# Kernel tuning notes

Measured on AMD Instinct MI355X. Metric: run time of the kernel, lower is better.

Reference implementation:

```python
import jax, jax.numpy as jnp
import numpy as np

NUM_EMB = 1000
HIDDEN = 256
SCALE = 2
N_HEADS = 8
HEAD_DIM = HIDDEN * SCALE // N_HEADS  # 64
HS = HIDDEN * SCALE  # 512
EPS = 1e-6


def setup_inputs() -> dict:
    key = jax.random.key(0)
    ks = jax.random.split(key, 12)
    B, N, C, H, W = 8, 8, HIDDEN, 32, 32
    std = 0.02
    return {
        "q": jax.random.randint(ks[0], (B,), 0, NUM_EMB, dtype=jnp.int32),
        "c": jax.random.normal(ks[1], (B, N, C, H, W), dtype=jnp.float32),
        "rms_w": jnp.ones((HIDDEN,), dtype=jnp.float32),
        "emb": jax.random.normal(ks[2], (NUM_EMB, HIDDEN), dtype=jnp.float32) * std,
        "w1": jax.random.normal(ks[3], (HIDDEN, HS), dtype=jnp.float32) * std,
        "b1": jnp.zeros((HS,), dtype=jnp.float32),
        "w2": jax.random.normal(ks[4], (HS, HS), dtype=jnp.float32) * std,
        "b2": jnp.zeros((HS,), dtype=jnp.float32),
        "w_kv": jax.random.normal(ks[5], (HIDDEN, HS * 2), dtype=jnp.float32) * std,
        "w_out": jax.random.normal(ks[6], (HS, HIDDEN), dtype=jnp.float32) * std,
        "b_out": jnp.zeros((HIDDEN,), dtype=jnp.float32),
    }


def reference(q, c, rms_w, emb, w1, b1, w2, b2, w_kv, w_out, b_out):
    B, N, C, H, W = c.shape
    attn_scale = HEAD_DIM ** (-0.5)
    # permute to [B,H,W,N,C] and RMSNorm over channel dim
    c = jnp.transpose(c, (0, 3, 4, 1, 2))
    c = c * jax.lax.rsqrt(jnp.mean(c * c, axis=-1, keepdims=True) + EPS) * rms_w
    # query path: embed + gated MLP -> [B, n_heads, head_dim]
    qe = emb[q]                                   # [B, hidden]
    qh = jax.nn.silu(qe @ w1 + b1) @ w2 + b2      # [B, HS]
    qh = qh.reshape(B, N_HEADS, HEAD_DIM)
    # kv projection: [B,H,W,N, 2*HS] -> [B,H,W,n_heads,N, 2*head_dim]
    kv = (c @ w_kv).reshape(B, H, W, N, N_HEADS, 2 * HEAD_DIM)
    kv = jnp.transpose(kv, (0, 1, 2, 4, 3, 5))
    k, v = jnp.split(kv, 2, axis=-1)              # each [B,H,W,heads,N,head_dim]
    # broadcast per-pixel cross-attention: query shared over H,W
    dots = jnp.einsum('bed,bhwend->bhwen', qh, k) * attn_scale
    attn = jax.nn.softmax(dots, axis=-1)
    h = jnp.einsum('bhwen,bhwend->bhwed', attn, v)  # [B,H,W,heads,head_dim]
    h = h.reshape(B, H, W, HS)
    out = h @ w_out + b_out                        # [B,H,W,hidden]
    return jnp.transpose(out, (0, 3, 1, 2))        # [B,hidden,H,W]
```

## Files before the change

kernel.cpp:

```cpp
#include <hip/hip_runtime.h>

typedef _Float16 f16;
typedef _Float16 f16x4 __attribute__((ext_vector_type(4)));
typedef _Float16 f16x8 __attribute__((ext_vector_type(8)));
typedef float f32x4 __attribute__((ext_vector_type(4)));

static __device__ inline char* a_addr(char* Abase, int px, int k) {
    return Abase + px * 4096 + ((((k >> 3) ^ (px & 15)) << 4) | ((k & 7) << 1));
}

__launch_bounds__(256)
__global__ void k_setup(const int* __restrict__ q, const float* __restrict__ emb,
                        const float* __restrict__ w1, const float* __restrict__ b1,
                        const float* __restrict__ w2, const float* __restrict__ b2,
                        const float* __restrict__ w_kv, const float* __restrict__ w_out,
                        const float* __restrict__ rms_w,
                        f16* __restrict__ qkw, f16* __restrict__ mtp) {
    int blk = blockIdx.x;
    int t = threadIdx.x;
    __shared__ float qe[256];
    __shared__ float x1L[512];
    __shared__ float ps[4][64];
    __shared__ float qhL[64];
    __shared__ float wv[64][8];

    if (blk < 64) {
        int b = blk >> 3, e = blk & 7;
        qe[t] = emb[(size_t)q[b] * 256 + t];
        __syncthreads();
        float a0 = b1[t], a1 = b1[t + 256];
#pragma unroll 4
        for (int c = 0; c < 256; ++c) {
            float qv = qe[c];
            a0 += qv * w1[c * 512 + t];
            a1 += qv * w1[c * 512 + t + 256];
        }
        x1L[t]       = a0 / (1.f + __expf(-a0));
        x1L[t + 256] = a1 / (1.f + __expf(-a1));
        __syncthreads();
        int d = t & 63, ks = t >> 6;
        float acc = 0.f;
#pragma unroll 4
        for (int k = ks * 128; k < ks * 128 + 128; ++k)
            acc += x1L[k] * w2[k * 512 + e * 64 + d];
        ps[ks][d] = acc;
        __syncthreads();
        if (t < 64)
            qhL[t] = b2[e * 64 + t] + ps[0][t] + ps[1][t] + ps[2][t] + ps[3][t];
        __syncthreads();
        const float* row = w_kv + (size_t)t * 1024 + e * 128;
        float a2 = 0.f;
#pragma unroll
        for (int dd = 0; dd < 64; dd += 4) {
            float4 wv4 = *(const float4*)(row + dd);
            a2 += qhL[dd] * wv4.x + qhL[dd + 1] * wv4.y + qhL[dd + 2] * wv4.z + qhL[dd + 3] * wv4.w;
        }
        qkw[(b * 8 + e) * 256 + t] = (f16)(a2 * rms_w[t]);
    } else {
        int mb = blk - 64;
        int e = mb >> 5, c0 = (mb & 31) * 8;
        {
            int d = t & 63, cc = t >> 6;
            wv[d][cc]     = w_kv[(size_t)(c0 + cc) * 1024 + e * 128 + 64 + d];
            wv[d][cc + 4] = w_kv[(size_t)(c0 + cc + 4) * 1024 + e * 128 + 64 + d];
        }
        __syncthreads();
        int o = t;
        float acc[8];
#pragma unroll
        for (int c = 0; c < 8; ++c) acc[c] = 0.f;
#pragma unroll 4
        for (int d = 0; d < 64; ++d) {
            float wo = w_out[(size_t)(e * 64 + d) * 256 + o];
            float4 wa = *(const float4*)&wv[d][0];
            float4 wb = *(const float4*)&wv[d][4];
            acc[0] += wa.x * wo; acc[1] += wa.y * wo; acc[2] += wa.z * wo; acc[3] += wa.w * wo;
            acc[4] += wb.x * wo; acc[5] += wb.y * wo; acc[6] += wb.z * wo; acc[7] += wb.w * wo;
        }
        f16x8 ov;
#pragma unroll
        for (int c = 0; c < 8; ++c) ov[c] = (f16)(acc[c] * rms_w[c0 + c]);
        *(f16x8*)(mtp + ((size_t)((e * 256 + c0) >> 3) * 256 + o) * 8) = ov;
    }
}

__launch_bounds__(1024, 4)
__global__ void k_attn(const float* __restrict__ cin, const f16* __restrict__ qkw,
                       const f16* __restrict__ mtp, const float* __restrict__ b_out,
                       float* __restrict__ out) {
    int blk = blockIdx.x;
    int b = blk & 7;
    int hw0 = (blk >> 3) * 32;
    int t = threadIdx.x;
    int lane = t & 63, w = t >> 6;
    int m16 = lane & 15, quad = lane >> 4;
    int half = lane >> 5;

    __shared__ char A[32 * 4096];
    __shared__ float dotsP[8][8][32];
    __shared__ float wredS[16][16];
    __shared__ f16  attnH[8 * 32 * 8];

    int n = w & 7, pxh = w >> 3;
    int px = pxh * 16 + m16;
    {
        const float* cb0 = cin + (((size_t)b * 2048) << 10) + hw0 + px;
        int chb = n * 256 + quad * 64;
        float ss = 0.f;
#pragma unroll
        for (int g = 0; g < 4; ++g) {
            float v[16];
#pragma unroll
            for (int j = 0; j < 16; ++j)
                v[j] = cb0[(size_t)(chb + g * 16 + j) << 10];
            f16x8 h0, h1;
#pragma unroll
            for (int j = 0; j < 8; ++j) { ss += v[j] * v[j]; h0[j] = (f16)v[j]; }
#pragma unroll
            for (int j = 0; j < 8; ++j) { float x = v[8 + j]; ss += x * x; h1[j] = (f16)x; }
            *(f16x8*)a_addr(A, px, chb + g * 16)     = h0;
            *(f16x8*)a_addr(A, px, chb + g * 16 + 8) = h1;
        }
        ss += __shfl_xor(ss, 16);
        ss += __shfl_xor(ss, 32);
        if (lane < 16) wredS[w][m16] = ss;
    }
    {
        f32x4 d0 = {0.f, 0.f, 0.f, 0.f};
        const f16* qrow = qkw + (size_t)b * 2048 + (m16 & 7) * 256;
#pragma unroll
        for (int ks = 0; ks < 8; ++ks) {
            f16x8 a0 = *(const f16x8*)a_addr(A, px, n * 256 + ks * 32 + quad * 8);
            f16x8 bq = *(const f16x8*)(qrow + ks * 32 + quad * 8);
            d0 = __builtin_amdgcn_mfma_f32_16x16x32_f16(a0, bq, d0, 0, 0, 0);
        }
        if (m16 < 8) {
#pragma unroll
            for (int r = 0; r < 4; ++r) dotsP[n][m16][pxh * 16 + quad * 4 + r] = d0[r];
        }
    }
    __syncthreads();

    int o = w * 16 + m16;
    f16x8 pb[8];
#pragma unroll
    for (int ks = 0; ks < 8; ++ks)
        pb[ks] = *(const f16x8*)(mtp + ((size_t)(ks * 4 + quad) * 256 + o) * 8);

    if (t < 256) {
        int e = t >> 5, p = t & 31;
        int ph = p >> 4, pl = p & 15;
        float rv[8], l[8];
#pragma unroll
        for (int nn = 0; nn < 8; ++nn)
            rv[nn] = rsqrtf(wredS[ph * 8 + nn][pl] * (1.f / 256.f) + 1e-6f);
#pragma unroll
        for (int nn = 0; nn < 8; ++nn) l[nn] = dotsP[nn][e][p] * rv[nn] * 0.125f;
        float mx = l[0];
#pragma unroll
        for (int nn = 1; nn < 8; ++nn) mx = fmaxf(mx, l[nn]);
        float s = 0.f;
#pragma unroll
        for (int nn = 0; nn < 8; ++nn) { l[nn] = __expf(l[nn] - mx); s += l[nn]; }
        float inv = 1.f / s;
        f16x8 av;
#pragma unroll
        for (int nn = 0; nn < 8; ++nn) av[nn] = (f16)(l[nn] * inv * rv[nn]);
        *(f16x8*)(attnH + e * 256 + p * 8) = av;
    }
    __syncthreads();

    {
        int bpx = lane & 31;
        int c0 = (w + half * 16) * 8;
        f16x8 cv[8];
#pragma unroll
        for (int nn = 0; nn < 8; ++nn)
            cv[nn] = *(const f16x8*)a_addr(A, bpx, nn * 256 + c0);
#pragma unroll
        for (int e = 0; e < 8; ++e) {
            f16x8 av = *(const f16x8*)(attnH + e * 256 + bpx * 8);
            f16x8 r = {};
#pragma unroll
            for (int nn = 0; nn < 8; ++nn) {
                f16 an = av[nn];
#pragma unroll
                for (int j = 0; j < 8; ++j) r[j] += cv[nn][j] * an;
            }
            *(f16x8*)a_addr(A, bpx, e * 256 + c0) = r;
        }
    }
    __syncthreads();

    {
        f32x4 acc0 = {0.f, 0.f, 0.f, 0.f};
        f32x4 acc1 = {0.f, 0.f, 0.f, 0.f};
#pragma unroll
        for (int ks = 0; ks < 8; ++ks) {
            int k = ks * 32 + quad * 8;
            f16x8 af0 = *(const f16x8*)a_addr(A, m16, k);
            f16x8 af1 = *(const f16x8*)a_addr(A, m16 + 16, k);
            acc0 = __builtin_amdgcn_mfma_f32_16x16x32_f16(af0, pb[ks], acc0, 0, 0, 0);
            acc1 = __builtin_amdgcn_mfma_f32_16x16x32_f16(af1, pb[ks], acc1, 0, 0, 0);
        }
#pragma unroll 8
        for (int ks = 8; ks < 64; ++ks) {
            int k = (ks >> 3) * 256 + (ks & 7) * 32 + quad * 8;
            int kchunk = k >> 3;
            f16x8 bfr = *(const f16x8*)(mtp + ((size_t)kchunk * 256 + o) * 8);
            f16x8 af0 = *(const f16x8*)a_addr(A, m16, k);
            f16x8 af1 = *(const f16x8*)a_addr(A, m16 + 16, k);
            acc0 = __builtin_amdgcn_mfma_f32_16x16x32_f16(af0, bfr, acc0, 0, 0, 0);
            acc1 = __builtin_amdgcn_mfma_f32_16x16x32_f16(af1, bfr, acc1, 0, 0, 0);
        }
        float bo = b_out[o];
        float* drow = out + ((size_t)b * 256 + o) * 1024 + hw0;
        float4 v0 = {acc0[0] + bo, acc0[1] + bo, acc0[2] + bo, acc0[3] + bo};
        float4 v1 = {acc1[0] + bo, acc1[1] + bo, acc1[2] + bo, acc1[3] + bo};
        *(float4*)(drow + quad * 4)      = v0;
        *(float4*)(drow + 16 + quad * 4) = v1;
    }
}

extern "C" void kernel_launch(void* const* d_in, const int* in_sizes, int n_in,
                              void* d_out, int out_size, void* d_ws, size_t ws_size,
                              hipStream_t stream) {
    (void)in_sizes; (void)n_in; (void)out_size; (void)ws_size;
    const int*   q     = (const int*)d_in[0];
    const float* c     = (const float*)d_in[1];
    const float* rms_w = (const float*)d_in[2];
    const float* emb   = (const float*)d_in[3];
    const float* w1    = (const float*)d_in[4];
    const float* b1    = (const float*)d_in[5];
    const float* w2    = (const float*)d_in[6];
    const float* b2    = (const float*)d_in[7];
    const float* w_kv  = (const float*)d_in[8];
    const float* w_out = (const float*)d_in[9];
    const float* b_out = (const float*)d_in[10];
    float* out = (float*)d_out;

    char* ws = (char*)d_ws;
    f16* qkw = (f16*)ws;
    f16* mtp = (f16*)(ws + 32768);

    k_setup<<<320, 256, 0, stream>>>(q, emb, w1, b1, w2, b2, w_kv, w_out, rms_w, qkw, mtp);
    k_attn <<<256, 1024, 0, stream>>>(c, qkw, mtp, b_out, out);
}
```

Baseline: 168.0 us.

## Fuse setup into attention kernel with grid-wide flag barrier and overlapped loads

Merges the weight-preprocessing kernel into the attention kernel. The first four warps of each block compute the folded w_kv·w_out slice and, in 64 blocks, the query MLP chain. The remaining warps stream the input tile into shared memory at the same time. A global atomic counter barrier, reset by a memset, makes every block wait until all qkw and mtp data is published. The aim is to remove one launch and hide the setup latency behind the input loads. The cost is a grid-wide spin wait, which relies on all 256 blocks being co-resident, and fewer warps doing the input loads.

```diff
diff --git a/kernel.cpp b/kernel.cpp
--- a/kernel.cpp
+++ b/kernel.cpp
@@ -5,89 +5,23 @@
 typedef _Float16 f16x8 __attribute__((ext_vector_type(8)));
 typedef float f32x4 __attribute__((ext_vector_type(4)));
 
+#define WS_QKW   0
+#define WS_MTP   32768
+#define WS_FLAGS (32768 + 1048576)
+
 static __device__ inline char* a_addr(char* Abase, int px, int k) {
     return Abase + px * 4096 + ((((k >> 3) ^ (px & 15)) << 4) | ((k & 7) << 1));
 }
 
-__launch_bounds__(256)
-__global__ void k_setup(const int* __restrict__ q, const float* __restrict__ emb,
+__launch_bounds__(1024, 4)
+__global__ void k_fused(const int* __restrict__ q, const float* __restrict__ emb,
                         const float* __restrict__ w1, const float* __restrict__ b1,
                         const float* __restrict__ w2, const float* __restrict__ b2,
                         const float* __restrict__ w_kv, const float* __restrict__ w_out,
-                        const float* __restrict__ rms_w,
-                        f16* __restrict__ qkw, f16* __restrict__ mtp) {
-    int blk = blockIdx.x;
-    int t = threadIdx.x;
-    __shared__ float qe[256];
-    __shared__ float x1L[512];
-    __shared__ float ps[4][64];
-    __shared__ float qhL[64];
-    __shared__ float wv[64][8];
-
-    if (blk < 64) {
-        int b = blk >> 3, e = blk & 7;
-        qe[t] = emb[(size_t)q[b] * 256 + t];
-        __syncthreads();
-        float a0 = b1[t], a1 = b1[t + 256];
-#pragma unroll 4
-        for (int c = 0; c < 256; ++c) {
-            float qv = qe[c];
-            a0 += qv * w1[c * 512 + t];
-            a1 += qv * w1[c * 512 + t + 256];
-        }
-        x1L[t]       = a0 / (1.f + __expf(-a0));
-        x1L[t + 256] = a1 / (1.f + __expf(-a1));
-        __syncthreads();
-        int d = t & 63, ks = t >> 6;
-        float acc = 0.f;
-#pragma unroll 4
-        for (int k = ks * 128; k < ks * 128 + 128; ++k)
-            acc += x1L[k] * w2[k * 512 + e * 64 + d];
-        ps[ks][d] = acc;
-        __syncthreads();
-        if (t < 64)
-            qhL[t] = b2[e * 64 + t] + ps[0][t] + ps[1][t] + ps[2][t] + ps[3][t];
-        __syncthreads();
-        const float* row = w_kv + (size_t)t * 1024 + e * 128;
-        float a2 = 0.f;
-#pragma unroll
-        for (int dd = 0; dd < 64; dd += 4) {
-            float4 wv4 = *(const float4*)(row + dd);
-            a2 += qhL[dd] * wv4.x + qhL[dd + 1] * wv4.y + qhL[dd + 2] * wv4.z + qhL[dd + 3] * wv4.w;
-        }
-        qkw[(b * 8 + e) * 256 + t] = (f16)(a2 * rms_w[t]);
-    } else {
-        int mb = blk - 64;
-        int e = mb >> 5, c0 = (mb & 31) * 8;
-        {
-            int d = t & 63, cc = t >> 6;
-            wv[d][cc]     = w_kv[(size_t)(c0 + cc) * 1024 + e * 128 + 64 + d];
-            wv[d][cc + 4] = w_kv[(size_t)(c0 + cc + 4) * 1024 + e * 128 + 64 + d];
-        }
-        __syncthreads();
-        int o = t;
-        float acc[8];
-#pragma unroll
-        for (int c = 0; c < 8; ++c) acc[c] = 0.f;
-#pragma unroll 4
-        for (int d = 0; d < 64; ++d) {
-            float wo = w_out[(size_t)(e * 64 + d) * 256 + o];
-            float4 wa = *(const float4*)&wv[d][0];
-            float4 wb = *(const float4*)&wv[d][4];
-            acc[0] += wa.x * wo; acc[1] += wa.y * wo; acc[2] += wa.z * wo; acc[3] += wa.w * wo;
-            acc[4] += wb.x * wo; acc[5] += wb.y * wo; acc[6] += wb.z * wo; acc[7] += wb.w * wo;
-        }
-        f16x8 ov;
-#pragma unroll
-        for (int c = 0; c < 8; ++c) ov[c] = (f16)(acc[c] * rms_w[c0 + c]);
-        *(f16x8*)(mtp + ((size_t)((e * 256 + c0) >> 3) * 256 + o) * 8) = ov;
-    }
-}
-
-__launch_bounds__(1024, 4)
-__global__ void k_attn(const float* __restrict__ cin, const f16* __restrict__ qkw,
-                       const f16* __restrict__ mtp, const float* __restrict__ b_out,
-                       float* __restrict__ out) {
+                        const float* __restrict__ rms_w, const float* __restrict__ cin,
+                        const float* __restrict__ b_out,
+                        f16* __restrict__ qkw, f16* __restrict__ mtp,
+                        int* __restrict__ flags, float* __restrict__ out) {
     int blk = blockIdx.x;
     int b = blk & 7;
     int hw0 = (blk >> 3) * 32;
@@ -97,42 +31,159 @@
     int half = lane >> 5;
 
     __shared__ char A[32 * 4096];
-    __shared__ float dotsP[8][8][32];
+    __shared__ __align__(16) char poolA[8192];
     __shared__ float wredS[16][16];
-    __shared__ f16  attnH[8 * 32 * 8];
-
-    int n = w & 7, pxh = w >> 3;
-    int px = pxh * 16 + m16;
+    __shared__ __align__(16) f16 attnH[2048];
+
+    float (*dotsP)[8][32] = (float (*)[8][32])poolA;
+    float* wvF  = (float*)poolA;
+    float* qeF  = (float*)(poolA + 2048);
+    float* x1LF = (float*)(poolA + 3072);
+    float* psF  = (float*)(poolA + 5120);
+    float* qhLF = (float*)(poolA + 6144);
+
+    bool chainblk = (blk < 64);
+    int bq = blk >> 3, eq = blk & 7;
+    int em = blk >> 5, c0m = (blk & 31) * 8;
+
+    int lw = w - 4;
+    int c1 = lw, c2 = 12 + lw;
+    float ss1 = 0.f, ss2 = 0.f;
+
+#define LOADP(c, p, ss)                                                         \
+    {                                                                           \
+        int pxh_ = (c) >> 3, n_ = (c) & 7;                                      \
+        int px_ = pxh_ * 16 + m16;                                              \
+        const float* cb0_ = cin + (((size_t)b) << 21) + hw0 + px_;              \
+        int chb_ = n_ * 256 + quad * 64 + (p) * 16;                             \
+        float v_[16];                                                           \
+        _Pragma("unroll")                                                       \
+        for (int j = 0; j < 16; ++j) v_[j] = cb0_[(size_t)(chb_ + j) << 10];    \
+        f16x8 h0_, h1_;                                                         \
+        _Pragma("unroll")                                                       \
+        for (int j = 0; j < 8; ++j) { ss += v_[j] * v_[j]; h0_[j] = (f16)v_[j]; } \
+        _Pragma("unroll")                                                       \
+        for (int j = 0; j < 8; ++j) { float x_ = v_[8 + j]; ss += x_ * x_; h1_[j] = (f16)x_; } \
+        *(f16x8*)a_addr(A, px_, chb_)     = h0_;                                \
+        *(f16x8*)a_addr(A, px_, chb_ + 8) = h1_;                                \
+    }
+
+    if (w < 4) {
+        int d = t & 63, cc = t >> 6;
+        wvF[d * 8 + cc]     = w_kv[(size_t)(c0m + cc) * 1024 + em * 128 + 64 + d];
+        wvF[d * 8 + cc + 4] = w_kv[(size_t)(c0m + cc + 4) * 1024 + em * 128 + 64 + d];
+        if (chainblk) qeF[t] = emb[(size_t)q[bq] * 256 + t];
+    } else {
+        LOADP(c1, 0, ss1);
+        if (lw < 4) LOADP(c2, 0, ss2);
+    }
+    __syncthreads();
+
+    if (w < 4) {
+        int o = t;
+        float acc[8];
+#pragma unroll
+        for (int c = 0; c < 8; ++c) acc[c] = 0.f;
+#pragma unroll 4
+        for (int d = 0; d < 64; ++d) {
+            float wo = w_out[(size_t)(em * 64 + d) * 256 + o];
+            float4 wa = *(const float4*)&wvF[d * 8];
+            float4 wb = *(const float4*)&wvF[d * 8 + 4];
+            acc[0] += wa.x * wo; acc[1] += wa.y * wo; acc[2] += wa.z * wo; acc[3] += wa.w * wo;
+            acc[4] += wb.x * wo; acc[5] += wb.y * wo; acc[6] += wb.z * wo; acc[7] += wb.w * wo;
+        }
+        f16x8 ov;
+#pragma unroll
+        for (int c = 0; c < 8; ++c) ov[c] = (f16)(acc[c] * rms_w[c0m + c]);
+        *(f16x8*)(mtp + ((size_t)((em * 256 + c0m) >> 3) * 256 + o) * 8) = ov;
+        __threadfence();
+    } else {
+        LOADP(c1, 1, ss1);
+        if (lw < 4) LOADP(c2, 1, ss2);
+    }
+    __syncthreads();
+
+    if (t == 0)
+        __hip_atomic_fetch_add(&flags[1], 1, __ATOMIC_RELEASE, __HIP_MEMORY_SCOPE_AGENT);
+    if (w < 4) {
+        if (chainblk) {
+            float a0 = b1[t], a1 = b1[t + 256];
+#pragma unroll 4
+            for (int c = 0; c < 256; ++c) {
+                float qv = qeF[c];
+                a0 += qv * w1[c * 512 + t];
+                a1 += qv * w1[c * 512 + t + 256];
+            }
+            x1LF[t]       = a0 / (1.f + __expf(-a0));
+            x1LF[t + 256] = a1 / (1.f + __expf(-a1));
+        }
+    } else {
+        LOADP(c1, 2, ss1);
+        if (lw < 4) LOADP(c2, 2, ss2);
+    }
+    __syncthreads();
+
+    if (w < 4) {
+        if (chainblk) {
+            int d = t & 63, ks = t >> 6;
+            float acc = 0.f;
+#pragma unroll 4
+            for (int k = ks * 128; k < ks * 128 + 128; ++k)
+                acc += x1LF[k] * w2[k * 512 + eq * 64 + d];
+            psF[ks * 64 + d] = acc;
+        }
+    } else {
+        LOADP(c1, 3, ss1);
+        if (lw < 4) LOADP(c2, 3, ss2);
+    }
+    __syncthreads();
+
+    if (w >= 4) {
+        ss1 += __shfl_xor(ss1, 16);
+        ss1 += __shfl_xor(ss1, 32);
+        if (lane < 16) wredS[c1][m16] = ss1;
+        if (lw < 4) {
+            ss2 += __shfl_xor(ss2, 16);
+            ss2 += __shfl_xor(ss2, 32);
+            if (lane < 16) wredS[c2][m16] = ss2;
+        }
+    } else if (chainblk && t < 64) {
+        qhLF[t] = b2[eq * 64 + t] + psF[t] + psF[64 + t] + psF[128 + t] + psF[192 + t];
+    }
+    __syncthreads();
+
+    if (chainblk && w < 4) {
+        const float* row = w_kv + (size_t)t * 1024 + eq * 128;
+        float a2 = 0.f;
+#pragma unroll
+        for (int dd = 0; dd < 64; dd += 4) {
+            float4 wv4 = *(const float4*)(row + dd);
+            a2 += qhLF[dd] * wv4.x + qhLF[dd + 1] * wv4.y
+                + qhLF[dd + 2] * wv4.z + qhLF[dd + 3] * wv4.w;
+        }
+        qkw[(bq * 8 + eq) * 256 + t] = (f16)(a2 * rms_w[t]);
+        __threadfence();
+    }
+    __syncthreads();
+
+    if (chainblk && t == 0)
+        __hip_atomic_fetch_add(&flags[0], 1, __ATOMIC_RELEASE, __HIP_MEMORY_SCOPE_AGENT);
+    if (t == 0) {
+        while (__hip_atomic_load(&flags[0], __ATOMIC_ACQUIRE, __HIP_MEMORY_SCOPE_AGENT) < 64 ||
+               __hip_atomic_load(&flags[1], __ATOMIC_ACQUIRE, __HIP_MEMORY_SCOPE_AGENT) < 256)
+            __builtin_amdgcn_s_sleep(2);
+    }
+    __syncthreads();
+
     {
-        const float* cb0 = cin + (((size_t)b * 2048) << 10) + hw0 + px;
-        int chb = n * 256 + quad * 64;
-        float ss = 0.f;
-#pragma unroll
-        for (int g = 0; g < 4; ++g) {
-            float v[16];
-#pragma unroll
-            for (int j = 0; j < 16; ++j)
-                v[j] = cb0[(size_t)(chb + g * 16 + j) << 10];
-            f16x8 h0, h1;
-#pragma unroll
-            for (int j = 0; j < 8; ++j) { ss += v[j] * v[j]; h0[j] = (f16)v[j]; }
-#pragma unroll
-            for (int j = 0; j < 8; ++j) { float x = v[8 + j]; ss += x * x; h1[j] = (f16)x; }
-            *(f16x8*)a_addr(A, px, chb + g * 16)     = h0;
-            *(f16x8*)a_addr(A, px, chb + g * 16 + 8) = h1;
-        }
-        ss += __shfl_xor(ss, 16);
-        ss += __shfl_xor(ss, 32);
-        if (lane < 16) wredS[w][m16] = ss;
-    }
-    {
+        int n = w & 7, pxh = w >> 3;
         f32x4 d0 = {0.f, 0.f, 0.f, 0.f};
         const f16* qrow = qkw + (size_t)b * 2048 + (m16 & 7) * 256;
 #pragma unroll
         for (int ks = 0; ks < 8; ++ks) {
-            f16x8 a0 = *(const f16x8*)a_addr(A, px, n * 256 + ks * 32 + quad * 8);
-            f16x8 bq = *(const f16x8*)(qrow + ks * 32 + quad * 8);
-            d0 = __builtin_amdgcn_mfma_f32_16x16x32_f16(a0, bq, d0, 0, 0, 0);
+            f16x8 a0 = *(const f16x8*)a_addr(A, pxh * 16 + m16, n * 256 + ks * 32 + quad * 8);
+            f16x8 bfr = *(const f16x8*)(qrow + ks * 32 + quad * 8);
+            d0 = __builtin_amdgcn_mfma_f32_16x16x32_f16(a0, bfr, d0, 0, 0, 0);
         }
         if (m16 < 8) {
 #pragma unroll
@@ -153,7 +204,7 @@
         float rv[8], l[8];
 #pragma unroll
         for (int nn = 0; nn < 8; ++nn)
-            rv[nn] = rsqrtf(wredS[ph * 8 + nn][pl] * (1.f / 256.f) + 1e-6f);
+            rv[nn] = rsqrtf(wredS[(ph << 3) | nn][pl] * (1.f / 256.f) + 1e-6f);
 #pragma unroll
         for (int nn = 0; nn < 8; ++nn) l[nn] = dotsP[nn][e][p] * rv[nn] * 0.125f;
         float mx = l[0];
@@ -220,6 +271,7 @@
         *(float4*)(drow + quad * 4)      = v0;
         *(float4*)(drow + 16 + quad * 4) = v1;
     }
+#undef LOADP
 }
 
 extern "C" void kernel_launch(void* const* d_in, const int* in_sizes, int n_in,
@@ -240,9 +292,11 @@
     float* out = (float*)d_out;
 
     char* ws = (char*)d_ws;
-    f16* qkw = (f16*)ws;
-    f16* mtp = (f16*)(ws + 32768);
-
-    k_setup<<<320, 256, 0, stream>>>(q, emb, w1, b1, w2, b2, w_kv, w_out, rms_w, qkw, mtp);
-    k_attn <<<256, 1024, 0, stream>>>(c, qkw, mtp, b_out, out);
+    f16* qkw   = (f16*)(ws + WS_QKW);
+    f16* mtp   = (f16*)(ws + WS_MTP);
+    int* flags = (int*)(ws + WS_FLAGS);
+
+    hipMemsetAsync(flags, 0, 64, stream);
+    k_fused<<<256, 1024, 0, stream>>>(q, emb, w1, b1, w2, b2, w_kv, w_out, rms_w,
+                                      c, b_out, qkw, mtp, flags, out);
 }
```

Measured after the change: 323.3 us. 92.4% more time.
